# Kernel optimization log

Hardware: AMD Instinct MI355X
Metric: run time of the kernel (lower is better)

The kernel has to match this reference:

```python
import jax, jax.numpy as jnp
import numpy as np

B, T, D, H, O, L = 64, 512, 256, 512, 1, 4


def _lstm_layer(x, W_ih, W_hh, b_ih, b_hh):
    """Single LSTM layer, batch_first. x: [B,T,in] -> [B,T,H].
    PyTorch gate order: i, f, g, o."""
    Bv = x.shape[0]
    Hv = W_hh.shape[1]
    # Precompute input contribution for all timesteps (one big GEMM).
    gx = jnp.einsum('btd,gd->btg', x, W_ih) + b_ih + b_hh  # [B,T,4H]

    def step(carry, g_t):
        h, c = carry
        z = g_t + h @ W_hh.T  # [B,4H]
        i, f, g, o = jnp.split(z, 4, axis=-1)
        i = jax.nn.sigmoid(i)
        f = jax.nn.sigmoid(f)
        g = jnp.tanh(g)
        o = jax.nn.sigmoid(o)
        c = f * c + i * g
        h = o * jnp.tanh(c)
        return (h, c), h

    h0 = jnp.zeros((Bv, Hv), x.dtype)
    c0 = jnp.zeros((Bv, Hv), x.dtype)
    _, hs = jax.lax.scan(step, (h0, c0), jnp.swapaxes(gx, 0, 1))  # [T,B,H]
    return jnp.swapaxes(hs, 0, 1)  # [B,T,H]


def setup_inputs() -> dict:
    key = jax.random.key(0)
    ks = jax.random.split(key, 19)
    s = 1.0 / np.sqrt(H)  # PyTorch LSTM init scale
    d = {"x": jax.random.normal(ks[0], (B, T, D), jnp.float32)}
    dims = [D, H, H, H]
    i = 1
    for l in range(L):
        d[f"W_ih{l}"] = jax.random.normal(ks[i], (4 * H, dims[l]), jnp.float32) * s; i += 1
        d[f"W_hh{l}"] = jax.random.normal(ks[i], (4 * H, H), jnp.float32) * s; i += 1
        d[f"b_ih{l}"] = jax.random.normal(ks[i], (4 * H,), jnp.float32) * s; i += 1
        d[f"b_hh{l}"] = jax.random.normal(ks[i], (4 * H,), jnp.float32) * s; i += 1
    d["W_out"] = jax.random.normal(ks[17], (O, H), jnp.float32) * s
    d["b_out"] = jax.random.normal(ks[18], (O,), jnp.float32) * s
    return d


def reference(x, W_ih0, W_hh0, b_ih0, b_hh0,
              W_ih1, W_hh1, b_ih1, b_hh1,
              W_ih2, W_hh2, b_ih2, b_hh2,
              W_ih3, W_hh3, b_ih3, b_hh3,
              W_out, b_out):
    h = x
    layers = ((W_ih0, W_hh0, b_ih0, b_hh0),
              (W_ih1, W_hh1, b_ih1, b_hh1),
              (W_ih2, W_hh2, b_ih2, b_hh2),
              (W_ih3, W_hh3, b_ih3, b_hh3))
    for Wih, Whh, bih, bhh in layers:
        h = _lstm_layer(h, Wih, Whh, bih, bhh)
    # Linear head on last timestep
    return h[:, -1, :] @ W_out.T + b_out  # [B, O]
```

## Files before the change

kernel.cpp:

```cpp
#include <hip/hip_runtime.h>
#include <hip/hip_fp16.h>

typedef _Float16 h16;
typedef _Float16 v8h  __attribute__((ext_vector_type(8)));
typedef float    v4f  __attribute__((ext_vector_type(4)));

#define FPAT 0x0101010101010101ull

struct PParams {
  const float* x;
  const float* Wih[4];
  const float* Whh[4];
  const float* bih[4];
  const float* bhh[4];
  h16* s[4];
  unsigned char* flags;
};

__device__ inline float fsigmoid(float x){
  float e = __builtin_amdgcn_exp2f(-1.4426950408889634f * __builtin_fabsf(x));
  float r = __builtin_amdgcn_rcpf(1.0f + e);
  return x >= 0.f ? r : e * r;
}
__device__ inline float ftanhf(float x){
  float e = __builtin_amdgcn_exp2f(-2.8853900817779268f * __builtin_fabsf(x));
  float t = (1.0f - e) * __builtin_amdgcn_rcpf(1.0f + e);
  return x >= 0.f ? t : -t;
}

__device__ inline unsigned long long cload64(const void* p){
  return __hip_atomic_load((const unsigned long long*)p, __ATOMIC_RELAXED,
                           __HIP_MEMORY_SCOPE_AGENT);
}
__device__ inline void cstore32(void* p, unsigned int v){
  __hip_atomic_store((unsigned int*)p, v, __ATOMIC_RELAXED, __HIP_MEMORY_SCOPE_AGENT);
}
__device__ inline void cstore8(void* p, unsigned char v){
  __hip_atomic_store((unsigned char*)p, v, __ATOMIC_RELAXED, __HIP_MEMORY_SCOPE_AGENT);
}

__device__ inline void wave_wait16(const unsigned long long* f, int lane){
  int it = 0;
  while (true){
    unsigned long long a = FPAT, b = FPAT;
    if (lane == 0){ a = cload64(f); b = cload64(f + 1); }
    if (__shfl((int)((a & b) == FPAT), 0, 64)) break;
    __builtin_amdgcn_s_sleep(1);
    if (++it > (1 << 21)) break;
  }
}

template<int KIN, bool XSRC, bool SAGENT>
__device__ void run_layer(const float* __restrict__ Wih, const float* __restrict__ Whh,
                          const float* __restrict__ bih, const float* __restrict__ bhh,
                          const float* __restrict__ xsrc,
                          const h16* __restrict__ src,
                          h16* __restrict__ dst, int dstMask,
                          unsigned char* flagSelf, const unsigned char* flagSrc,
                          int rg, int bg, h16* A)
{
  const int tid  = threadIdx.x;
  const int wv   = tid >> 6;
  const int lane = tid & 63;
  const int ISTR = KIN + 8;
  const int HOFF = 8320;
  const int KI   = KIN / 32;

  const int n16  = lane & 15;
  const int unit = rg*32 + wv*8 + (n16 & 7);
  const int ksub = ((lane >> 4) & 3) * 8;
  const int row0 = ((n16 >> 3)    ) * 512 + unit;
  const int row1 = ((n16 >> 3) + 2) * 512 + unit;

  v8h wihf[KI][2];
  #pragma unroll
  for (int kk = 0; kk < KI; ++kk){
    #pragma unroll
    for (int j = 0; j < 2; ++j){
      const float* p = Wih + (size_t)(j ? row1 : row0) * KIN + kk*32 + ksub;
      v8h fr;
      #pragma unroll
      for (int e = 0; e < 8; ++e) fr[e] = (h16)p[e];
      wihf[kk][j] = fr;
    }
  }
  v8h whhf[16][2];
  #pragma unroll
  for (int kk = 0; kk < 16; ++kk){
    #pragma unroll
    for (int j = 0; j < 2; ++j){
      const float* p = Whh + (size_t)(j ? row1 : row0) * 512 + kk*32 + ksub;
      v8h fr;
      #pragma unroll
      for (int e = 0; e < 8; ++e) fr[e] = (h16)p[e];
      whhf[kk][j] = fr;
    }
  }
  const float bias0 = bih[row0] + bhh[row0];
  const float bias1 = bih[row1] + bhh[row1];
  float c[4] = {0.f, 0.f, 0.f, 0.f};
  const bool hi = (lane & 8) != 0;

  #pragma unroll 1
  for (int t = 0; t < 512; ++t){
    if constexpr (!XSRC)
      wave_wait16((const unsigned long long*)(flagSrc + (size_t)t*16), lane);

    if constexpr (XSRC){
      #pragma unroll
      for (int i = 0; i < 2; ++i){
        int q = tid + i*256;
        int row = q >> 5, col = q & 31;
        const float* xp = xsrc + ((size_t)(bg*16 + row)*512 + t)*256 + col*8;
        float4 v0 = *(const float4*)(xp);
        float4 v1 = *(const float4*)(xp + 4);
        v8h o = {(h16)v0.x,(h16)v0.y,(h16)v0.z,(h16)v0.w,
                 (h16)v1.x,(h16)v1.y,(h16)v1.z,(h16)v1.w};
        *(v8h*)(A + row*ISTR + col*8) = o;
      }
    } else {
      v8h hv[4];
      #pragma unroll
      for (int i = 0; i < 4; ++i){
        int q = tid + i*256;
        int row = q >> 6, col = q & 63;
        hv[i] = *(const v8h*)(src + ((size_t)t*64 + bg*16 + row)*512 + col*8);
      }
      #pragma unroll
      for (int i = 0; i < 4; ++i){
        int q = tid + i*256;
        int row = q >> 6, col = q & 63;
        *(v8h*)(A + row*ISTR + col*8) = hv[i];
      }
    }
    __syncthreads();

    unsigned long long pa = FPAT, pb = FPAT;
    const unsigned long long* fsPrev =
        (const unsigned long long*)(flagSelf + (size_t)(t-1)*16);
    if (t > 0 && lane == 0){
      pa = cload64(fsPrev);
      pb = cload64(fsPrev + 1);
    }

    v4f a0e = {0.f,0.f,0.f,0.f}, a0o = {0.f,0.f,0.f,0.f};
    v4f a1e = {0.f,0.f,0.f,0.f}, a1o = {0.f,0.f,0.f,0.f};
    const h16* Ain = A + n16*ISTR + ksub;
    #pragma unroll
    for (int kk = 0; kk < KI; ++kk){
      v8h a = *(const v8h*)(Ain + kk*32);
      if (kk & 1){
        a0o = __builtin_amdgcn_mfma_f32_16x16x32_f16(a, wihf[kk][0], a0o, 0, 0, 0);
        a1o = __builtin_amdgcn_mfma_f32_16x16x32_f16(a, wihf[kk][1], a1o, 0, 0, 0);
      } else {
        a0e = __builtin_amdgcn_mfma_f32_16x16x32_f16(a, wihf[kk][0], a0e, 0, 0, 0);
        a1e = __builtin_amdgcn_mfma_f32_16x16x32_f16(a, wihf[kk][1], a1e, 0, 0, 0);
      }
    }

    if (t > 0){
      if (!__shfl((int)((pa & pb) == FPAT), 0, 64))
        wave_wait16(fsPrev, lane);
    }

    if (t == 0){
      #pragma unroll
      for (int i = 0; i < 4; ++i){
        int q = tid + i*256;
        int row = q >> 6, col = q & 63;
        union { unsigned long long u[2]; v8h h; } tmp;
        tmp.u[0] = 0ull; tmp.u[1] = 0ull;
        *(v8h*)(A + HOFF + row*520 + col*8) = tmp.h;
      }
    } else if constexpr (SAGENT){
      const h16* hsrc = dst + (size_t)((t-1) & dstMask) * 64 * 512;
      unsigned long long a0[4], a1[4];
      #pragma unroll
      for (int i = 0; i < 4; ++i){
        int q = tid + i*256;
        int row = q >> 6, col = q & 63;
        const h16* sp = hsrc + (size_t)(bg*16 + row)*512 + col*8;
        a0[i] = cload64(sp);
        a1[i] = cload64(sp + 4);
      }
      #pragma unroll
      for (int i = 0; i < 4; ++i){
        int q = tid + i*256;
        int row = q >> 6, col = q & 63;
        union { unsigned long long u[2]; v8h h; } tmp;
        tmp.u[0] = a0[i]; tmp.u[1] = a1[i];
        *(v8h*)(A + HOFF + row*520 + col*8) = tmp.h;
      }
    } else {
      const h16* hsrc = dst + (size_t)((t-1) & dstMask) * 64 * 512;
      v8h hv[4];
      #pragma unroll
      for (int i = 0; i < 4; ++i){
        int q = tid + i*256;
        int row = q >> 6, col = q & 63;
        hv[i] = *(const v8h*)(hsrc + (size_t)(bg*16 + row)*512 + col*8);
      }
      #pragma unroll
      for (int i = 0; i < 4; ++i){
        int q = tid + i*256;
        int row = q >> 6, col = q & 63;
        *(v8h*)(A + HOFF + row*520 + col*8) = hv[i];
      }
    }
    __syncthreads();

    const h16* Ah = A + HOFF + n16*520 + ksub;
    #pragma unroll
    for (int kk = 0; kk < 16; ++kk){
      v8h a = *(const v8h*)(Ah + kk*32);
      if (kk & 1){
        a0o = __builtin_amdgcn_mfma_f32_16x16x32_f16(a, whhf[kk][0], a0o, 0, 0, 0);
        a1o = __builtin_amdgcn_mfma_f32_16x16x32_f16(a, whhf[kk][1], a1o, 0, 0, 0);
      } else {
        a0e = __builtin_amdgcn_mfma_f32_16x16x32_f16(a, whhf[kk][0], a0e, 0, 0, 0);
        a1e = __builtin_amdgcn_mfma_f32_16x16x32_f16(a, whhf[kk][1], a1e, 0, 0, 0);
      }
    }

    h16* drow = dst + (size_t)(t & dstMask) * 64 * 512;
    #pragma unroll
    for (int r = 0; r < 4; ++r){
      float z0 = a0e[r] + a0o[r] + bias0;
      float z1 = a1e[r] + a1o[r] + bias1;
      float p0 = __shfl_xor(z0, 8, 64);
      float p1 = __shfl_xor(z1, 8, 64);
      float iv = hi ? p0 : z0;
      float fv = hi ? z0 : p0;
      float gv = hi ? p1 : z1;
      float ov = hi ? z1 : p1;
      iv = fsigmoid(iv); fv = fsigmoid(fv); ov = fsigmoid(ov);
      gv = ftanhf(gv);
      c[r] = fv * c[r] + iv * gv;
      float hval = ov * ftanhf(c[r]);
      h16 hh = (h16)hval;
      unsigned int mine = (unsigned int)__builtin_bit_cast(unsigned short, hh);
      unsigned int partner = (unsigned int)__shfl_xor((int)mine, 1, 64);
      if (!hi && !(n16 & 1)){
        int batch = bg*16 + ((lane >> 4) << 2) + r;
        cstore32((void*)(drow + (size_t)batch*512 + unit), mine | (partner << 16));
      }
    }
    __syncthreads();

    if (tid == 0)
      cstore8(flagSelf + (size_t)t*16 + rg, 1);
  }
}

__global__ __launch_bounds__(256, 1) void lstm_persist(PParams p){
  __shared__ h16 A[16640];
  const int bx = blockIdx.x;
  const int l  = bx >> 6;
  const int rg = (bx >> 2) & 15;
  const int bg = bx & 3;
  unsigned char* fl = p.flags + (size_t)(l*4 + bg) * 512 * 16;
  if (l == 0){
    run_layer<256, true,  false>(p.Wih[0], p.Whh[0], p.bih[0], p.bhh[0], p.x, nullptr,
                                 p.s[0], 511, fl, nullptr, rg, bg, A);
  } else if (l < 3){
    const unsigned char* fs = p.flags + (size_t)((l-1)*4 + bg) * 512 * 16;
    run_layer<512, false, false>(p.Wih[l], p.Whh[l], p.bih[l], p.bhh[l], nullptr,
                                 p.s[l-1], p.s[l], 511, fl, fs, rg, bg, A);
  } else {
    const unsigned char* fs = p.flags + (size_t)(2*4 + bg) * 512 * 16;
    run_layer<512, false, true >(p.Wih[3], p.Whh[3], p.bih[3], p.bhh[3], nullptr,
                                 p.s[2], p.s[3], 1, fl, fs, rg, bg, A);
  }
}

__global__ void head_k(const h16* __restrict__ h3, const float* __restrict__ Wo,
                       const float* __restrict__ bo, float* __restrict__ out){
  const int b = blockIdx.x;
  const int lane = threadIdx.x;
  float s = 0.f;
  for (int u = lane; u < 512; u += 64)
    s += (float)h3[(size_t)b * 512 + u] * Wo[u];
  #pragma unroll
  for (int off = 32; off; off >>= 1) s += __shfl_down(s, off, 64);
  if (lane == 0) out[b] = s + bo[0];
}

__global__ void zero_out_k(float* out, int n){
  int i = blockIdx.x * 64 + threadIdx.x;
  if (i < n) out[i] = 0.f;
}

extern "C" void kernel_launch(void* const* d_in, const int* in_sizes, int n_in,
                              void* d_out, int out_size, void* d_ws, size_t ws_size,
                              hipStream_t stream){
  PParams p;
  p.x = (const float*)d_in[0];
  for (int l = 0; l < 4; ++l){
    p.Wih[l] = (const float*)d_in[1 + 4*l + 0];
    p.Whh[l] = (const float*)d_in[1 + 4*l + 1];
    p.bih[l] = (const float*)d_in[1 + 4*l + 2];
    p.bhh[l] = (const float*)d_in[1 + 4*l + 3];
  }
  const float* Wo = (const float*)d_in[17];
  const float* bo = (const float*)d_in[18];

  const size_t FLAG_BYTES = (size_t)16 * 512 * 16;
  const size_t SBYTES     = (size_t)512 * 64 * 512 * 2;
  const size_t NEED       = FLAG_BYTES + 3 * SBYTES + (size_t)2 * 64 * 512 * 2;

  if (ws_size < NEED){
    zero_out_k<<<dim3(1), dim3(64), 0, stream>>>((float*)d_out, out_size);
    return;
  }

  char* ws = (char*)d_ws;
  p.flags = (unsigned char*)ws;
  size_t off = FLAG_BYTES;
  for (int l = 0; l < 3; ++l){ p.s[l] = (h16*)(ws + off); off += SBYTES; }
  p.s[3] = (h16*)(ws + off);

  hipMemsetAsync(p.flags, 0, FLAG_BYTES, stream);

  void* args[] = { &p };
  hipError_t e = hipLaunchCooperativeKernel((void*)lstm_persist, dim3(256), dim3(256),
                                            args, 0, stream);
  if (e != hipSuccess){
    lstm_persist<<<dim3(256), dim3(256), 0, stream>>>(p);
  }

  head_k<<<dim3(64), dim3(64), 0, stream>>>(p.s[3] + (size_t)64 * 512, Wo, bo, (float*)d_out);
}
```

Measured before the change: 1.909 ms.

## Replace per-block step flags with per-wave flags and wave-local h loading

Each wave now publishes its own completion flag per timestep, dropping the trailing block barrier. The h-state gather is remapped so each wave waits only on the quad of 16 producer flags covering the 128 columns it loads, rather than on every block. Cross-layer consumers poll 64 flags instead of 16. This is meant to shorten the critical path of the recurrent dependency chain, at the cost of more flag traffic and a larger flag buffer.

```diff
diff --git a/kernel.cpp b/kernel.cpp
--- a/kernel.cpp
+++ b/kernel.cpp
@@ -45,6 +45,16 @@
     unsigned long long a = FPAT, b = FPAT;
     if (lane == 0){ a = cload64(f); b = cload64(f + 1); }
     if (__shfl((int)((a & b) == FPAT), 0, 64)) break;
+    __builtin_amdgcn_s_sleep(1);
+    if (++it > (1 << 21)) break;
+  }
+}
+__device__ inline void wave_wait64(const unsigned long long* f, int lane){
+  int it = 0;
+  while (true){
+    unsigned long long a = FPAT, b = FPAT, c = FPAT, d = FPAT;
+    if (lane == 0){ a = cload64(f); b = cload64(f+1); c = cload64(f+2); d = cload64(f+3); }
+    if (__shfl((int)(((a & b) & (c & d)) == FPAT), 0, 64)) break;
     __builtin_amdgcn_s_sleep(1);
     if (++it > (1 << 21)) break;
   }
@@ -72,6 +82,9 @@
   const int row0 = ((n16 >> 3)    ) * 512 + unit;
   const int row1 = ((n16 >> 3) + 2) * 512 + unit;
 
+  const int qrow = lane >> 4;
+  const int qoff = 128*wv + (lane & 15)*8;
+
   v8h wihf[KI][2];
   #pragma unroll
   for (int kk = 0; kk < KI; ++kk){
@@ -104,7 +117,7 @@
   #pragma unroll 1
   for (int t = 0; t < 512; ++t){
     if constexpr (!XSRC)
-      wave_wait16((const unsigned long long*)(flagSrc + (size_t)t*16), lane);
+      wave_wait64((const unsigned long long*)(flagSrc + (size_t)t*64), lane);
 
     if constexpr (XSRC){
       #pragma unroll
@@ -136,11 +149,11 @@
     __syncthreads();
 
     unsigned long long pa = FPAT, pb = FPAT;
-    const unsigned long long* fsPrev =
-        (const unsigned long long*)(flagSelf + (size_t)(t-1)*16);
+    const unsigned long long* fsQuad =
+        (const unsigned long long*)(flagSelf + (size_t)(t-1)*64 + wv*16);
     if (t > 0 && lane == 0){
-      pa = cload64(fsPrev);
-      pb = cload64(fsPrev + 1);
+      pa = cload64(fsQuad);
+      pb = cload64(fsQuad + 1);
     }
 
     v4f a0e = {0.f,0.f,0.f,0.f}, a0o = {0.f,0.f,0.f,0.f};
@@ -160,52 +173,40 @@
 
     if (t > 0){
       if (!__shfl((int)((pa & pb) == FPAT), 0, 64))
-        wave_wait16(fsPrev, lane);
+        wave_wait16(fsQuad, lane);
     }
 
     if (t == 0){
       #pragma unroll
-      for (int i = 0; i < 4; ++i){
-        int q = tid + i*256;
-        int row = q >> 6, col = q & 63;
+      for (int j = 0; j < 4; ++j){
         union { unsigned long long u[2]; v8h h; } tmp;
         tmp.u[0] = 0ull; tmp.u[1] = 0ull;
-        *(v8h*)(A + HOFF + row*520 + col*8) = tmp.h;
+        *(v8h*)(A + HOFF + (qrow + 4*j)*520 + qoff) = tmp.h;
       }
     } else if constexpr (SAGENT){
       const h16* hsrc = dst + (size_t)((t-1) & dstMask) * 64 * 512;
       unsigned long long a0[4], a1[4];
       #pragma unroll
-      for (int i = 0; i < 4; ++i){
-        int q = tid + i*256;
-        int row = q >> 6, col = q & 63;
-        const h16* sp = hsrc + (size_t)(bg*16 + row)*512 + col*8;
-        a0[i] = cload64(sp);
-        a1[i] = cload64(sp + 4);
-      }
-      #pragma unroll
-      for (int i = 0; i < 4; ++i){
-        int q = tid + i*256;
-        int row = q >> 6, col = q & 63;
+      for (int j = 0; j < 4; ++j){
+        const h16* sp = hsrc + (size_t)(bg*16 + qrow + 4*j)*512 + qoff;
+        a0[j] = cload64(sp);
+        a1[j] = cload64(sp + 4);
+      }
+      #pragma unroll
+      for (int j = 0; j < 4; ++j){
         union { unsigned long long u[2]; v8h h; } tmp;
-        tmp.u[0] = a0[i]; tmp.u[1] = a1[i];
-        *(v8h*)(A + HOFF + row*520 + col*8) = tmp.h;
+        tmp.u[0] = a0[j]; tmp.u[1] = a1[j];
+        *(v8h*)(A + HOFF + (qrow + 4*j)*520 + qoff) = tmp.h;
       }
     } else {
       const h16* hsrc = dst + (size_t)((t-1) & dstMask) * 64 * 512;
       v8h hv[4];
       #pragma unroll
-      for (int i = 0; i < 4; ++i){
-        int q = tid + i*256;
-        int row = q >> 6, col = q & 63;
-        hv[i] = *(const v8h*)(hsrc + (size_t)(bg*16 + row)*512 + col*8);
-      }
-      #pragma unroll
-      for (int i = 0; i < 4; ++i){
-        int q = tid + i*256;
-        int row = q >> 6, col = q & 63;
-        *(v8h*)(A + HOFF + row*520 + col*8) = hv[i];
-      }
+      for (int j = 0; j < 4; ++j)
+        hv[j] = *(const v8h*)(hsrc + (size_t)(bg*16 + qrow + 4*j)*512 + qoff);
+      #pragma unroll
+      for (int j = 0; j < 4; ++j)
+        *(v8h*)(A + HOFF + (qrow + 4*j)*520 + qoff) = hv[j];
     }
     __syncthreads();
 
@@ -245,10 +246,10 @@
         cstore32((void*)(drow + (size_t)batch*512 + unit), mine | (partner << 16));
       }
     }
-    __syncthreads();
-
-    if (tid == 0)
-      cstore8(flagSelf + (size_t)t*16 + rg, 1);
+
+    asm volatile("s_waitcnt vmcnt(0)" ::: "memory");
+    if (lane == 0)
+      cstore8(flagSelf + (size_t)t*64 + (rg*4 + wv), 1);
   }
 }
 
@@ -258,16 +259,16 @@
   const int l  = bx >> 6;
   const int rg = (bx >> 2) & 15;
   const int bg = bx & 3;
-  unsigned char* fl = p.flags + (size_t)(l*4 + bg) * 512 * 16;
+  unsigned char* fl = p.flags + (size_t)(l*4 + bg) * 512 * 64;
   if (l == 0){
     run_layer<256, true,  false>(p.Wih[0], p.Whh[0], p.bih[0], p.bhh[0], p.x, nullptr,
                                  p.s[0], 511, fl, nullptr, rg, bg, A);
   } else if (l < 3){
-    const unsigned char* fs = p.flags + (size_t)((l-1)*4 + bg) * 512 * 16;
+    const unsigned char* fs = p.flags + (size_t)((l-1)*4 + bg) * 512 * 64;
     run_layer<512, false, false>(p.Wih[l], p.Whh[l], p.bih[l], p.bhh[l], nullptr,
                                  p.s[l-1], p.s[l], 511, fl, fs, rg, bg, A);
   } else {
-    const unsigned char* fs = p.flags + (size_t)(2*4 + bg) * 512 * 16;
+    const unsigned char* fs = p.flags + (size_t)(2*4 + bg) * 512 * 64;
     run_layer<512, false, true >(p.Wih[3], p.Whh[3], p.bih[3], p.bhh[3], nullptr,
                                  p.s[2], p.s[3], 1, fl, fs, rg, bg, A);
   }
@@ -304,7 +305,7 @@
   const float* Wo = (const float*)d_in[17];
   const float* bo = (const float*)d_in[18];
 
-  const size_t FLAG_BYTES = (size_t)16 * 512 * 16;
+  const size_t FLAG_BYTES = (size_t)16 * 512 * 64;
   const size_t SBYTES     = (size_t)512 * 64 * 512 * 2;
   const size_t NEED       = FLAG_BYTES + 3 * SBYTES + (size_t)2 * 64 * 512 * 2;
 
```

New measurement: 2.610 ms. 36.7% more time.
